# Kernel tuning notes

Hardware: AMD Instinct MI355X
Metric: run time of the kernel (lower is better)

Reference implementation:

```python
import jax, jax.numpy as jnp
import numpy as np

H, B, I = 1024, 64, 128
W_SCALE = 0.192
BETA = 10.0 / W_SCALE   # softplus-like sharpness 'b' in source
DT = 0.1
DELTA_T = 1.0
Z_MIN, Z_MAX = 0.001, 0.1


def setup_inputs() -> dict:
    key = jax.random.key(0)
    ks = jax.random.split(key, 12)
    s = 1.0 / np.sqrt(H)  # nn.init.uniform_(param, -1/sqrt(H), 1/sqrt(H))
    u = lambda k, shp: jax.random.uniform(k, shp, jnp.float32, -s, s)
    return {
        "x": jax.random.normal(ks[0], (I, B), jnp.float32),
        "v_t": jnp.zeros((B, H), jnp.float32),
        "X": jnp.ones((B, H, H), jnp.float32),            # depression state x=1
        "U": jnp.full((B, H, H), 0.9, jnp.float32),       # facilitation state U=0.9
        "raw_w_r": u(ks[1], (H, H)),
        "p_r": u(ks[2], (H, I)),
        "b_r": u(ks[3], (H, 1)),
        "g_z": u(ks[4], (H, 1)),
        "c_x": u(ks[5], (H, H)),
        "c_u": u(ks[6], (H, H)),
        "c_U": u(ks[7], (H, H)),
        "a_exc": jax.random.uniform(ks[8], (), jnp.float32, -s, s),
        "a_inh": jax.random.uniform(ks[9], (), jnp.float32, -s, s),
    }


def reference(x, v_t, X, U, raw_w_r, p_r, b_r, g_z, c_x, c_u, c_U, a_exc, a_inh):
    sig = jax.nn.sigmoid
    # rectified recurrent weights: (1/b) * log(cosh(b * raw)) -- same formula in
    # all four quadrants of the source, so apply it to the whole matrix.
    w_r = jnp.log(jnp.cosh(BETA * raw_w_r)) / BETA          # (H, H), >= 0
    w_z = jnp.abs(w_r)
    p_z = jnp.abs(p_r)
    # Dale gain: excitatory gain for first half of rows, inhibitory for second.
    a = jnp.concatenate([jnp.full((H // 2, 1), 1.0) * a_exc,
                         jnp.full((H // 2, 1), 1.0) * a_inh], axis=0)
    A = 10.0 * sig(a)                                        # (H, 1)

    vt = v_t.T                                               # (H, B)
    r = sig(vt)                                              # (H, B) firing rates
    rb = r.T[:, :, None]                                     # (B, H, 1) -> r_t[j,b]

    # synaptic depression X: X' = z_x + (1-z_x)X - dt * U * X * r_pre
    z_x = Z_MIN + (Z_MAX - Z_MIN) * sig(c_x)                 # (H, H)
    X_new = z_x + (1.0 - z_x) * X - DELTA_T * U * (X * rb)   # (B, H, H)

    # synaptic facilitation U: U' = Ucap*z_u + (1-z_u)U + dt * Ucap * (1-U) * r_pre
    z_u = Z_MIN + (Z_MAX - Z_MIN) * sig(c_u)
    Ucap = 0.9 * sig(c_U)                                    # (H, H)
    U_new = Ucap * z_u + (1.0 - z_u) * U + DELTA_T * Ucap * ((1.0 - U) * rb)
    U_new = jnp.clip(U_new, jax.lax.stop_gradient(Ucap)[None], 1.0)

    # gate z_t = dt * sigmoid(w_z (A*r) + p_z x + g_z)
    z_t = DT * sig(w_z @ (A * r) + p_z @ x + g_z)            # (H, B)

    # membrane update: per-batch effective weights (X*U*w_r) applied to rates
    rec = jnp.einsum('bjk,kb->jb', X_new * U_new * w_r, r)   # (H, B)
    v_new = (1.0 - z_t) * vt + DT * (rec + p_r @ x + b_r)    # (H, B)
    v_new = v_new.T                                          # (B, H)

    return v_new
```

## Files before the change

kernel.cpp:

```cpp
#include <hip/hip_runtime.h>
#include <cstddef>

#define Hdim 1024
#define Bdim 64
#define Idim 128

#define BETA_F 52.083333333333336f
#define INV_BETA_F 0.0192f
#define LN2_F 0.6931471805599453f

__device__ __forceinline__ float sigf(float x) {
    return 1.0f / (1.0f + __expf(-x));
}

__device__ __forceinline__ float logcoshf_(float t) {
    float a = fabsf(t);
    return a + log1pf(__expf(-2.0f * a)) - LN2_F;
}

__global__ void pre_kernel(const float* __restrict__ x,
                           const float* __restrict__ v_t,
                           const float* __restrict__ p_r,
                           const float* __restrict__ b_r,
                           const float* __restrict__ g_z,
                           float* __restrict__ r_ws,
                           float* __restrict__ membx,
                           float* __restrict__ gatex) {
    const int j = blockIdx.x;
    const int b = threadIdx.x;
    const float* pr = p_r + (size_t)j * Idim;
    float accm = 0.0f, accg = 0.0f;
#pragma unroll 4
    for (int i = 0; i < Idim; ++i) {
        float p  = pr[i];
        float xv = x[i * Bdim + b];
        accm = fmaf(p, xv, accm);
        accg = fmaf(fabsf(p), xv, accg);
    }
    membx[j * Bdim + b] = accm + b_r[j];
    gatex[j * Bdim + b] = accg + g_z[j];

    int id = j * Bdim + b;
    r_ws[id] = sigf(v_t[id]);
}

__global__ __launch_bounds__(256, 4) void main_kernel(
    const float* __restrict__ X,
    const float* __restrict__ U,
    const float* __restrict__ raw_w_r,
    const float* __restrict__ c_x,
    const float* __restrict__ c_u,
    const float* __restrict__ c_U,
    const float* __restrict__ v_t,
    const float* __restrict__ a_exc,
    const float* __restrict__ a_inh,
    const float* __restrict__ r_ws,
    const float* __restrict__ membx,
    const float* __restrict__ gatex,
    float* __restrict__ out) {
    __shared__ __align__(16) float s_zx[Hdim];
    __shared__ __align__(16) float s_zu[Hdim];
    __shared__ __align__(16) float s_uc[Hdim];
    __shared__ __align__(16) float s_wr[Hdim];

    const int j     = blockIdx.x >> 1;
    const int bbase = (blockIdx.x & 1) * (Bdim / 2);
    const int tid   = threadIdx.x;

    const float Aexc = 10.0f * sigf(a_exc[0]);
    const float Ainh = 10.0f * sigf(a_inh[0]);

    {
        const int k = tid * 4;
        const size_t ro = (size_t)j * Hdim + k;
        float4 rw = *(const float4*)(raw_w_r + ro);
        float4 cx = *(const float4*)(c_x + ro);
        float4 cu = *(const float4*)(c_u + ro);
        float4 cN = *(const float4*)(c_U + ro);

        s_wr[k + 0] = logcoshf_(BETA_F * rw.x) * INV_BETA_F;
        s_wr[k + 1] = logcoshf_(BETA_F * rw.y) * INV_BETA_F;
        s_wr[k + 2] = logcoshf_(BETA_F * rw.z) * INV_BETA_F;
        s_wr[k + 3] = logcoshf_(BETA_F * rw.w) * INV_BETA_F;

        s_zx[k + 0] = 0.001f + 0.099f * sigf(cx.x);
        s_zx[k + 1] = 0.001f + 0.099f * sigf(cx.y);
        s_zx[k + 2] = 0.001f + 0.099f * sigf(cx.z);
        s_zx[k + 3] = 0.001f + 0.099f * sigf(cx.w);

        s_zu[k + 0] = 0.001f + 0.099f * sigf(cu.x);
        s_zu[k + 1] = 0.001f + 0.099f * sigf(cu.y);
        s_zu[k + 2] = 0.001f + 0.099f * sigf(cu.z);
        s_zu[k + 3] = 0.001f + 0.099f * sigf(cu.w);

        s_uc[k + 0] = 0.9f * sigf(cN.x);
        s_uc[k + 1] = 0.9f * sigf(cN.y);
        s_uc[k + 2] = 0.9f * sigf(cN.z);
        s_uc[k + 3] = 0.9f * sigf(cN.w);
    }
    __syncthreads();

    const int wave = tid >> 6;
    const int lane = tid & 63;

    for (int bo = wave; bo < Bdim / 2; bo += 4) {
        const int b = bbase + bo;
        const float* Xb = X + (size_t)b * Hdim * Hdim + (size_t)j * Hdim;
        const float* Ub = U + (size_t)b * Hdim * Hdim + (size_t)j * Hdim;
        const float* rb = r_ws + b * Hdim;
        const float rj = rb[j];

        float rec = 0.0f, gate = 0.0f;
#pragma unroll
        for (int it = 0; it < 4; ++it) {
            const float Ah = (it < 2) ? Aexc : Ainh;
            const int k = (it * 64 + lane) * 4;
            float4 Xv = *(const float4*)(Xb + k);
            float4 Uv = *(const float4*)(Ub + k);
            float4 rv = *(const float4*)(rb + k);
            float4 zx = *(const float4*)(s_zx + k);
            float4 zu = *(const float4*)(s_zu + k);
            float4 uc = *(const float4*)(s_uc + k);
            float4 wr = *(const float4*)(s_wr + k);

#define COMPONENT(c)                                                          \
    {                                                                         \
        float xn = zx.c + (1.0f - zx.c) * Xv.c - Uv.c * Xv.c * rj;            \
        float un = uc.c * zu.c + (1.0f - zu.c) * Uv.c +                       \
                   uc.c * (1.0f - Uv.c) * rj;                                 \
        un = fminf(fmaxf(un, uc.c), 1.0f);                                    \
        rec  = fmaf(xn * un * wr.c, rv.c, rec);                               \
        gate = fmaf(wr.c * Ah, rv.c, gate);                                   \
    }
            COMPONENT(x)
            COMPONENT(y)
            COMPONENT(z)
            COMPONENT(w)
#undef COMPONENT
        }

        const float vt = v_t[(size_t)b * Hdim + j];
        const float gx = gatex[j * Bdim + b];
        const float mx = membx[j * Bdim + b];

#pragma unroll
        for (int off = 32; off > 0; off >>= 1) {
            rec  += __shfl_xor(rec, off, 64);
            gate += __shfl_xor(gate, off, 64);
        }

        if (lane == 0) {
            float z  = 0.1f * sigf(gate + gx);
            float vn = (1.0f - z) * vt + 0.1f * (rec + mx);
            out[(size_t)b * Hdim + j] = vn;
        }
    }
}

extern "C" void kernel_launch(void* const* d_in, const int* in_sizes, int n_in,
                              void* d_out, int out_size, void* d_ws, size_t ws_size,
                              hipStream_t stream) {
    const float* x       = (const float*)d_in[0];
    const float* v_t     = (const float*)d_in[1];
    const float* X       = (const float*)d_in[2];
    const float* U       = (const float*)d_in[3];
    const float* raw_w_r = (const float*)d_in[4];
    const float* p_r     = (const float*)d_in[5];
    const float* b_r     = (const float*)d_in[6];
    const float* g_z     = (const float*)d_in[7];
    const float* c_x     = (const float*)d_in[8];
    const float* c_u     = (const float*)d_in[9];
    const float* c_U     = (const float*)d_in[10];
    const float* a_exc   = (const float*)d_in[11];
    const float* a_inh   = (const float*)d_in[12];

    float* out = (float*)d_out;

    float* r_ws  = (float*)d_ws;
    float* membx = r_ws + Bdim * Hdim;
    float* gatex = membx + Hdim * Bdim;

    pre_kernel<<<dim3(Hdim), dim3(Bdim), 0, stream>>>(
        x, v_t, p_r, b_r, g_z, r_ws, membx, gatex);

    main_kernel<<<dim3(Hdim * 2), dim3(256), 0, stream>>>(
        X, U, raw_w_r, c_x, c_u, c_U, v_t, a_exc, a_inh,
        r_ws, membx, gatex, out);
}
```

Measured before the change: 558.4 us.

## Double-buffer X/U rows into LDS via global_load_lds per wave

Each wave now streams its batch rows of X and U into a per-wave double-buffered LDS staging area with direct global-to-LDS loads, prefetching the next batch while computing the current one. The grid is halved so each block covers all 64 batches for one row j, which amortises the per-row setup (logcosh and sigmoid tables) over twice the work. This aims to hide HBM latency on the dominant 512MB stream. In exchange it adds 64KB of LDS per block, which lowers occupancy, and fewer blocks are launched.

```diff
diff --git a/kernel.cpp b/kernel.cpp
--- a/kernel.cpp
+++ b/kernel.cpp
@@ -1,5 +1,6 @@
 #include <hip/hip_runtime.h>
 #include <cstddef>
+#include <cstdint>
 
 #define Hdim 1024
 #define Bdim 64
@@ -16,6 +17,12 @@
 __device__ __forceinline__ float logcoshf_(float t) {
     float a = fabsf(t);
     return a + log1pf(__expf(-2.0f * a)) - LN2_F;
+}
+
+__device__ __forceinline__ void stage16(const float* gsrc, float* ldst) {
+    auto g = (const __attribute__((address_space(1))) uint32_t*)(uintptr_t)gsrc;
+    auto l = (__attribute__((address_space(3))) uint32_t*)(uint32_t)(uintptr_t)ldst;
+    __builtin_amdgcn_global_load_lds(g, l, 16, 0, 0);
 }
 
 __global__ void pre_kernel(const float* __restrict__ x,
@@ -62,10 +69,10 @@
     __shared__ __align__(16) float s_zu[Hdim];
     __shared__ __align__(16) float s_uc[Hdim];
     __shared__ __align__(16) float s_wr[Hdim];
-
-    const int j     = blockIdx.x >> 1;
-    const int bbase = (blockIdx.x & 1) * (Bdim / 2);
-    const int tid   = threadIdx.x;
+    __shared__ __align__(16) float s_stage[4][2][2048];
+
+    const int j   = blockIdx.x;
+    const int tid = threadIdx.x;
 
     const float Aexc = 10.0f * sigf(a_exc[0]);
     const float Ainh = 10.0f * sigf(a_inh[0]);
@@ -103,10 +110,32 @@
     const int wave = tid >> 6;
     const int lane = tid & 63;
 
-    for (int bo = wave; bo < Bdim / 2; bo += 4) {
-        const int b = bbase + bo;
-        const float* Xb = X + (size_t)b * Hdim * Hdim + (size_t)j * Hdim;
-        const float* Ub = U + (size_t)b * Hdim * Hdim + (size_t)j * Hdim;
+    float* const st0 = &s_stage[wave][0][0];
+    float* const st1 = &s_stage[wave][1][0];
+
+#define STAGE_BATCH(b_, buf_)                                                 \
+    {                                                                         \
+        const float* Xb_ = X + (size_t)(b_) * (Hdim * Hdim) + (size_t)j * Hdim;\
+        const float* Ub_ = U + (size_t)(b_) * (Hdim * Hdim) + (size_t)j * Hdim;\
+        _Pragma("unroll")                                                     \
+        for (int c_ = 0; c_ < 4; ++c_) {                                      \
+            stage16(Xb_ + c_ * 256 + lane * 4, (buf_) + c_ * 256);            \
+            stage16(Ub_ + c_ * 256 + lane * 4, (buf_) + 1024 + c_ * 256);     \
+        }                                                                     \
+    }
+
+    STAGE_BATCH(wave, st0)
+
+    for (int n = 0; n < 16; ++n) {
+        const int b = wave + n * 4;
+        float* cur = (n & 1) ? st1 : st0;
+        float* nxt = (n & 1) ? st0 : st1;
+
+        asm volatile("s_waitcnt vmcnt(0)" ::: "memory");
+        __builtin_amdgcn_sched_barrier(0);
+
+        if (n < 15) STAGE_BATCH(b + 4, nxt)
+
         const float* rb = r_ws + b * Hdim;
         const float rj = rb[j];
 
@@ -114,9 +143,9 @@
 #pragma unroll
         for (int it = 0; it < 4; ++it) {
             const float Ah = (it < 2) ? Aexc : Ainh;
-            const int k = (it * 64 + lane) * 4;
-            float4 Xv = *(const float4*)(Xb + k);
-            float4 Uv = *(const float4*)(Ub + k);
+            const int k = it * 256 + lane * 4;
+            float4 Xv = *(const float4*)(cur + k);
+            float4 Uv = *(const float4*)(cur + 1024 + k);
             float4 rv = *(const float4*)(rb + k);
             float4 zx = *(const float4*)(s_zx + k);
             float4 zu = *(const float4*)(s_zu + k);
@@ -155,6 +184,7 @@
             out[(size_t)b * Hdim + j] = vn;
         }
     }
+#undef STAGE_BATCH
 }
 
 extern "C" void kernel_launch(void* const* d_in, const int* in_sizes, int n_in,
@@ -183,7 +213,7 @@
     pre_kernel<<<dim3(Hdim), dim3(Bdim), 0, stream>>>(
         x, v_t, p_r, b_r, g_z, r_ws, membx, gatex);
 
-    main_kernel<<<dim3(Hdim * 2), dim3(256), 0, stream>>>(
+    main_kernel<<<dim3(Hdim), dim3(256), 0, stream>>>(
         X, U, raw_w_r, c_x, c_u, c_U, v_t, a_exc, a_inh,
         r_ws, membx, gatex, out);
 }
```

Result: no change. 556.3 us (-0.4%).

## Process two rows per block across the full batch in main kernel

Applied to the files above, without the earlier changes.

Each block now handles two output rows and all 64 batch entries instead of one row and half the batch. This halves the redundant per-row transform of the weights and gate parameters and shares the rate-vector loads between the two rows. Each iteration also issues more independent loads per wave. The grid shrinks to 512 blocks and the launch bounds are relaxed, which lowers occupancy and may hurt latency hiding.

```diff
diff --git a/kernel.cpp b/kernel.cpp
--- a/kernel.cpp
+++ b/kernel.cpp
@@ -1,5 +1,6 @@
 #include <hip/hip_runtime.h>
 #include <cstddef>
+#include <cstdint>
 
 #define Hdim 1024
 #define Bdim 64
@@ -44,7 +45,7 @@
     r_ws[id] = sigf(v_t[id]);
 }
 
-__global__ __launch_bounds__(256, 4) void main_kernel(
+__global__ __launch_bounds__(256, 2) void main_kernel(
     const float* __restrict__ X,
     const float* __restrict__ U,
     const float* __restrict__ raw_w_r,
@@ -58,72 +59,80 @@
     const float* __restrict__ membx,
     const float* __restrict__ gatex,
     float* __restrict__ out) {
-    __shared__ __align__(16) float s_zx[Hdim];
-    __shared__ __align__(16) float s_zu[Hdim];
-    __shared__ __align__(16) float s_uc[Hdim];
-    __shared__ __align__(16) float s_wr[Hdim];
-
-    const int j     = blockIdx.x >> 1;
-    const int bbase = (blockIdx.x & 1) * (Bdim / 2);
-    const int tid   = threadIdx.x;
+    __shared__ __align__(16) float s_zx[2][Hdim];
+    __shared__ __align__(16) float s_zu[2][Hdim];
+    __shared__ __align__(16) float s_uc[2][Hdim];
+    __shared__ __align__(16) float s_wr[2][Hdim];
+
+    const int j0  = blockIdx.x * 2;
+    const int tid = threadIdx.x;
 
     const float Aexc = 10.0f * sigf(a_exc[0]);
     const float Ainh = 10.0f * sigf(a_inh[0]);
 
-    {
-        const int k = tid * 4;
-        const size_t ro = (size_t)j * Hdim + k;
+#pragma unroll
+    for (int f = tid; f < 512; f += 256) {
+        const int row = f >> 8;
+        const int k   = (f & 255) * 4;
+        const size_t ro = (size_t)(j0 + row) * Hdim + k;
         float4 rw = *(const float4*)(raw_w_r + ro);
         float4 cx = *(const float4*)(c_x + ro);
         float4 cu = *(const float4*)(c_u + ro);
         float4 cN = *(const float4*)(c_U + ro);
 
-        s_wr[k + 0] = logcoshf_(BETA_F * rw.x) * INV_BETA_F;
-        s_wr[k + 1] = logcoshf_(BETA_F * rw.y) * INV_BETA_F;
-        s_wr[k + 2] = logcoshf_(BETA_F * rw.z) * INV_BETA_F;
-        s_wr[k + 3] = logcoshf_(BETA_F * rw.w) * INV_BETA_F;
-
-        s_zx[k + 0] = 0.001f + 0.099f * sigf(cx.x);
-        s_zx[k + 1] = 0.001f + 0.099f * sigf(cx.y);
-        s_zx[k + 2] = 0.001f + 0.099f * sigf(cx.z);
-        s_zx[k + 3] = 0.001f + 0.099f * sigf(cx.w);
-
-        s_zu[k + 0] = 0.001f + 0.099f * sigf(cu.x);
-        s_zu[k + 1] = 0.001f + 0.099f * sigf(cu.y);
-        s_zu[k + 2] = 0.001f + 0.099f * sigf(cu.z);
-        s_zu[k + 3] = 0.001f + 0.099f * sigf(cu.w);
-
-        s_uc[k + 0] = 0.9f * sigf(cN.x);
-        s_uc[k + 1] = 0.9f * sigf(cN.y);
-        s_uc[k + 2] = 0.9f * sigf(cN.z);
-        s_uc[k + 3] = 0.9f * sigf(cN.w);
+        s_wr[row][k + 0] = logcoshf_(BETA_F * rw.x) * INV_BETA_F;
+        s_wr[row][k + 1] = logcoshf_(BETA_F * rw.y) * INV_BETA_F;
+        s_wr[row][k + 2] = logcoshf_(BETA_F * rw.z) * INV_BETA_F;
+        s_wr[row][k + 3] = logcoshf_(BETA_F * rw.w) * INV_BETA_F;
+
+        s_zx[row][k + 0] = 0.001f + 0.099f * sigf(cx.x);
+        s_zx[row][k + 1] = 0.001f + 0.099f * sigf(cx.y);
+        s_zx[row][k + 2] = 0.001f + 0.099f * sigf(cx.z);
+        s_zx[row][k + 3] = 0.001f + 0.099f * sigf(cx.w);
+
+        s_zu[row][k + 0] = 0.001f + 0.099f * sigf(cu.x);
+        s_zu[row][k + 1] = 0.001f + 0.099f * sigf(cu.y);
+        s_zu[row][k + 2] = 0.001f + 0.099f * sigf(cu.z);
+        s_zu[row][k + 3] = 0.001f + 0.099f * sigf(cu.w);
+
+        s_uc[row][k + 0] = 0.9f * sigf(cN.x);
+        s_uc[row][k + 1] = 0.9f * sigf(cN.y);
+        s_uc[row][k + 2] = 0.9f * sigf(cN.z);
+        s_uc[row][k + 3] = 0.9f * sigf(cN.w);
     }
     __syncthreads();
 
     const int wave = tid >> 6;
     const int lane = tid & 63;
 
-    for (int bo = wave; bo < Bdim / 2; bo += 4) {
-        const int b = bbase + bo;
-        const float* Xb = X + (size_t)b * Hdim * Hdim + (size_t)j * Hdim;
-        const float* Ub = U + (size_t)b * Hdim * Hdim + (size_t)j * Hdim;
+    for (int b = wave; b < Bdim; b += 4) {
+        const float* Xb = X + (size_t)b * Hdim * Hdim + (size_t)j0 * Hdim;
+        const float* Ub = U + (size_t)b * Hdim * Hdim + (size_t)j0 * Hdim;
         const float* rb = r_ws + b * Hdim;
-        const float rj = rb[j];
-
-        float rec = 0.0f, gate = 0.0f;
-#pragma unroll
+        const float rj0 = rb[j0];
+        const float rj1 = rb[j0 + 1];
+
+        float rec0 = 0.0f, gate0 = 0.0f;
+        float rec1 = 0.0f, gate1 = 0.0f;
+#pragma unroll 2
         for (int it = 0; it < 4; ++it) {
             const float Ah = (it < 2) ? Aexc : Ainh;
-            const int k = (it * 64 + lane) * 4;
-            float4 Xv = *(const float4*)(Xb + k);
-            float4 Uv = *(const float4*)(Ub + k);
-            float4 rv = *(const float4*)(rb + k);
-            float4 zx = *(const float4*)(s_zx + k);
-            float4 zu = *(const float4*)(s_zu + k);
-            float4 uc = *(const float4*)(s_uc + k);
-            float4 wr = *(const float4*)(s_wr + k);
-
-#define COMPONENT(c)                                                          \
+            const int k = it * 256 + lane * 4;
+            float4 rv  = *(const float4*)(rb + k);
+            float4 Xv0 = *(const float4*)(Xb + k);
+            float4 Xv1 = *(const float4*)(Xb + Hdim + k);
+            float4 Uv0 = *(const float4*)(Ub + k);
+            float4 Uv1 = *(const float4*)(Ub + Hdim + k);
+            float4 zx0 = *(const float4*)(&s_zx[0][k]);
+            float4 zx1 = *(const float4*)(&s_zx[1][k]);
+            float4 zu0 = *(const float4*)(&s_zu[0][k]);
+            float4 zu1 = *(const float4*)(&s_zu[1][k]);
+            float4 uc0 = *(const float4*)(&s_uc[0][k]);
+            float4 uc1 = *(const float4*)(&s_uc[1][k]);
+            float4 wr0 = *(const float4*)(&s_wr[0][k]);
+            float4 wr1 = *(const float4*)(&s_wr[1][k]);
+
+#define COMPONENT(c, Xv, Uv, zx, zu, uc, wr, rj, rec, gate)                   \
     {                                                                         \
         float xn = zx.c + (1.0f - zx.c) * Xv.c - Uv.c * Xv.c * rj;            \
         float un = uc.c * zu.c + (1.0f - zu.c) * Uv.c +                       \
@@ -132,27 +141,39 @@
         rec  = fmaf(xn * un * wr.c, rv.c, rec);                               \
         gate = fmaf(wr.c * Ah, rv.c, gate);                                   \
     }
-            COMPONENT(x)
-            COMPONENT(y)
-            COMPONENT(z)
-            COMPONENT(w)
+            COMPONENT(x, Xv0, Uv0, zx0, zu0, uc0, wr0, rj0, rec0, gate0)
+            COMPONENT(y, Xv0, Uv0, zx0, zu0, uc0, wr0, rj0, rec0, gate0)
+            COMPONENT(z, Xv0, Uv0, zx0, zu0, uc0, wr0, rj0, rec0, gate0)
+            COMPONENT(w, Xv0, Uv0, zx0, zu0, uc0, wr0, rj0, rec0, gate0)
+            COMPONENT(x, Xv1, Uv1, zx1, zu1, uc1, wr1, rj1, rec1, gate1)
+            COMPONENT(y, Xv1, Uv1, zx1, zu1, uc1, wr1, rj1, rec1, gate1)
+            COMPONENT(z, Xv1, Uv1, zx1, zu1, uc1, wr1, rj1, rec1, gate1)
+            COMPONENT(w, Xv1, Uv1, zx1, zu1, uc1, wr1, rj1, rec1, gate1)
 #undef COMPONENT
         }
 
-        const float vt = v_t[(size_t)b * Hdim + j];
-        const float gx = gatex[j * Bdim + b];
-        const float mx = membx[j * Bdim + b];
+        const float vt0 = v_t[(size_t)b * Hdim + j0];
+        const float vt1 = v_t[(size_t)b * Hdim + j0 + 1];
+        const float gx0 = gatex[j0 * Bdim + b];
+        const float gx1 = gatex[(j0 + 1) * Bdim + b];
+        const float mx0 = membx[j0 * Bdim + b];
+        const float mx1 = membx[(j0 + 1) * Bdim + b];
 
 #pragma unroll
         for (int off = 32; off > 0; off >>= 1) {
-            rec  += __shfl_xor(rec, off, 64);
-            gate += __shfl_xor(gate, off, 64);
+            rec0  += __shfl_xor(rec0, off, 64);
+            gate0 += __shfl_xor(gate0, off, 64);
+            rec1  += __shfl_xor(rec1, off, 64);
+            gate1 += __shfl_xor(gate1, off, 64);
         }
 
         if (lane == 0) {
-            float z  = 0.1f * sigf(gate + gx);
-            float vn = (1.0f - z) * vt + 0.1f * (rec + mx);
-            out[(size_t)b * Hdim + j] = vn;
+            float z0 = 0.1f * sigf(gate0 + gx0);
+            out[(size_t)b * Hdim + j0] =
+                (1.0f - z0) * vt0 + 0.1f * (rec0 + mx0);
+            float z1 = 0.1f * sigf(gate1 + gx1);
+            out[(size_t)b * Hdim + j0 + 1] =
+                (1.0f - z1) * vt1 + 0.1f * (rec1 + mx1);
         }
     }
 }
@@ -183,7 +204,7 @@
     pre_kernel<<<dim3(Hdim), dim3(Bdim), 0, stream>>>(
         x, v_t, p_r, b_r, g_z, r_ws, membx, gatex);
 
-    main_kernel<<<dim3(Hdim * 2), dim3(256), 0, stream>>>(
+    main_kernel<<<dim3(Hdim / 2), dim3(256), 0, stream>>>(
         X, U, raw_w_r, c_x, c_u, c_U, v_t, a_exc, a_inh,
         r_ws, membx, gatex, out);
 }
```

Measured after the change: 549.0 us. No clear change (-1.7%).
